# Kernel tuning notes

Measured on AMD Instinct MI355X. Metric: run time of the kernel, lower is better.

Reference implementation:

```python
import jax, jax.numpy as jnp
import numpy as np

B, ENC, W = 256, 512, 256      # batch, encoder hidden (backbone_out), encoder width
ATTN, DEC, EMB, V = 256, 256, 128, 81  # attn_sz, dec_hs, emb_size, alphabet_size
T = 100                         # text_max_len


def setup_inputs() -> dict:
    key = jax.random.key(0)
    ks = jax.random.split(key, 15)
    s = 0.05
    return {
        "enc_out": jax.random.normal(ks[0], (B, ENC, W), jnp.float32),
        "emb": jax.random.normal(ks[1], (V, EMB), jnp.float32) * s,
        "enc_conv_w": jax.random.normal(ks[2], (ATTN, ENC), jnp.float32) * s,  # Conv1d k=1
        "enc_conv_b": jax.random.normal(ks[3], (ATTN,), jnp.float32) * s,
        "dec_lin_w": jax.random.normal(ks[4], (ATTN, DEC), jnp.float32) * s,
        "dec_lin_b": jax.random.normal(ks[5], (ATTN,), jnp.float32) * s,
        "energy_w": jax.random.normal(ks[6], (ATTN,), jnp.float32) * s,  # Conv1d attn->1, k=1
        "energy_b": jax.random.normal(ks[7], (1,), jnp.float32) * s,
        "w_ih": jax.random.normal(ks[8], (4 * DEC, EMB + ENC), jnp.float32) * s,
        "w_hh": jax.random.normal(ks[9], (4 * DEC, DEC), jnp.float32) * s,
        "b_ih": jax.random.normal(ks[10], (4 * DEC,), jnp.float32) * s,
        "b_hh": jax.random.normal(ks[11], (4 * DEC,), jnp.float32) * s,
        "out_w": jax.random.normal(ks[12], (V, DEC), jnp.float32) * s,
        "out_b": jax.random.normal(ks[13], (V,), jnp.float32) * s,
        "text_max_len": T,
        "sos_idx": 0,
    }


def reference(enc_out, emb, enc_conv_w, enc_conv_b, dec_lin_w, dec_lin_b,
              energy_w, energy_b, w_ih, w_hh, b_ih, b_hh, out_w, out_b,
              text_max_len, sos_idx):
    bs = enc_out.shape[0]
    dec_hs = w_hh.shape[1]
    # precompute encoder projection (Conv1d with kernel 1) once: [bs, attn, W]
    weighted_enc = jnp.einsum('bew,ae->baw', enc_out, enc_conv_w) + enc_conv_b[None, :, None]

    def step(carry, _):
        h, c, x = carry
        ex = emb[x]                                            # [bs, emb]
        dec_proj = h @ dec_lin_w.T + dec_lin_b                 # [bs, attn]
        pre = jnp.tanh(weighted_enc + dec_proj[:, :, None])    # [bs, attn, W]
        scores = jnp.einsum('baw,a->bw', pre, energy_w) + energy_b  # [bs, W]
        alphas = jax.nn.softmax(scores, axis=-1)
        context = jnp.einsum('bew,bw->be', enc_out, alphas)    # [bs, enc]
        rnn_x = jnp.concatenate([ex, context], axis=1)         # [bs, emb+enc]
        gates = rnn_x @ w_ih.T + b_ih + h @ w_hh.T + b_hh      # [bs, 4*dec]
        i, f, g, o = jnp.split(gates, 4, axis=1)               # torch LSTMCell gate order
        i, f, o = jax.nn.sigmoid(i), jax.nn.sigmoid(f), jax.nn.sigmoid(o)
        g = jnp.tanh(g)
        c_new = f * c + i * g
        h_new = o * jnp.tanh(c_new)
        logits = h_new @ out_w.T + out_b                       # [bs, V]
        logp = jax.nn.log_softmax(logits, axis=-1)
        nxt = jnp.argmax(logp, axis=-1).astype(jnp.int32)      # greedy feedback (eval mode)
        return (h_new, c_new, nxt), (logp, nxt, alphas)

    h0 = jnp.zeros((bs, dec_hs), enc_out.dtype)
    c0 = jnp.zeros((bs, dec_hs), enc_out.dtype)
    x0 = jnp.full((bs,), sos_idx, jnp.int32)
    _, (logps, preds, attns) = jax.lax.scan(step, (h0, c0, x0), None, length=text_max_len)
    # [T,bs,...] -> [bs,T,...]
    return (logps.transpose(1, 0, 2), preds.T, attns.transpose(1, 0, 2))
```

## Files before the change

### kernel.cpp

```cpp
#include <hip/hip_runtime.h>

#define BATCH 256
#define ENCH  512
#define WWID  256
#define ATT   256
#define DECH  256
#define EMBD  128
#define VOC   81
#define TT    100

__device__ __forceinline__ float ftanh(float x) {
  float e = expf(2.0f * x);
  return 1.0f - 2.0f / (e + 1.0f);
}
__device__ __forceinline__ float fsig(float x) {
  return 1.0f / (1.0f + expf(-x));
}

__global__ void k_build(const float* __restrict__ w_ih, const float* __restrict__ w_hh,
                        const float* __restrict__ dlw,
                        float* __restrict__ W2, float* __restrict__ DW2) {
  int k = blockIdx.x, tid = threadIdx.x;
  if (k < 768) {
    for (int g = tid; g < 1024; g += 256)
      W2[(size_t)k * 1024 + g] = (k < 512) ? w_ih[(size_t)g * 640 + 128 + k]
                                           : w_hh[(size_t)g * 256 + (k - 512)];
  } else {
    int kk = k - 768;
    DW2[kk * 256 + tid] = dlw[tid * 256 + kk];
  }
}

__global__ void k_embg(const float* __restrict__ emb, const float* __restrict__ w_ih,
                       const float* __restrict__ b_ih, const float* __restrict__ b_hh,
                       float* __restrict__ embg) {
  int v = blockIdx.x, tid = threadIdx.x;
  __shared__ float em[EMBD];
  if (tid < EMBD) em[tid] = emb[v * EMBD + tid];
  __syncthreads();
  for (int g = tid; g < 1024; g += 256) {
    float s = b_ih[g] + b_hh[g];
    const float* wr = w_ih + (size_t)g * 640;
#pragma unroll 8
    for (int e = 0; e < EMBD; ++e) s += em[e] * wr[e];
    embg[v * 1024 + g] = s;
  }
}

__global__ void __launch_bounds__(256) k_we(const float* __restrict__ enc,
                                            const float* __restrict__ cw,
                                            const float* __restrict__ cb,
                                            float* __restrict__ we) {
  int bid = blockIdx.x;
  int b = bid >> 4, at = (bid >> 2) & 3, wt = bid & 3;
  int a0 = at * 64, w0 = wt * 64;
  __shared__ float cwT[32][68];
  __shared__ float encT[32][64];
  int tid = threadIdx.x;
  int tx = tid & 15, ty = tid >> 4;
  float acc[4][4] = {};
  const float* encB = enc + (size_t)b * ENCH * WWID;
  for (int k0 = 0; k0 < ENCH; k0 += 32) {
    {
      int a = tid >> 2, e8 = (tid & 3) * 8;
      const float* src = cw + (size_t)(a0 + a) * ENCH + k0 + e8;
      float4 v0 = *(const float4*)(src);
      float4 v1 = *(const float4*)(src + 4);
      cwT[e8 + 0][a] = v0.x; cwT[e8 + 1][a] = v0.y; cwT[e8 + 2][a] = v0.z; cwT[e8 + 3][a] = v0.w;
      cwT[e8 + 4][a] = v1.x; cwT[e8 + 5][a] = v1.y; cwT[e8 + 6][a] = v1.z; cwT[e8 + 7][a] = v1.w;
    }
    {
      int e = tid >> 3, w8 = (tid & 7) * 8;
      const float* src = encB + (size_t)(k0 + e) * WWID + w0 + w8;
      *(float4*)&encT[e][w8] = *(const float4*)src;
      *(float4*)&encT[e][w8 + 4] = *(const float4*)(src + 4);
    }
    __syncthreads();
#pragma unroll
    for (int e = 0; e < 32; ++e) {
      float4 av = *(const float4*)&cwT[e][ty * 4];
      float4 bv = *(const float4*)&encT[e][tx * 4];
      float a4[4] = {av.x, av.y, av.z, av.w};
      float b4[4] = {bv.x, bv.y, bv.z, bv.w};
#pragma unroll
      for (int i = 0; i < 4; ++i)
#pragma unroll
        for (int j = 0; j < 4; ++j) acc[i][j] += a4[i] * b4[j];
    }
    __syncthreads();
  }
#pragma unroll
  for (int i = 0; i < 4; ++i) {
    int a = a0 + ty * 4 + i;
    float bias = cb[a];
    float4 o;
    o.x = acc[i][0] + bias; o.y = acc[i][1] + bias;
    o.z = acc[i][2] + bias; o.w = acc[i][3] + bias;
    *(float4*)(we + ((size_t)(b * ATT + a)) * WWID + w0 + tx * 4) = o;
  }
}

__global__ void __launch_bounds__(1024, 1) k_loop(
    const float* __restrict__ we, const float* __restrict__ enc,
    const float* __restrict__ W2, const float* __restrict__ DW2,
    const float* __restrict__ embg, const float* __restrict__ dlb,
    const float* __restrict__ ew, const float* __restrict__ eb,
    const float* __restrict__ ow, const float* __restrict__ ob,
    const int* __restrict__ sos, float* __restrict__ out) {
  const int tid = threadIdx.x;
  const int b = blockIdx.x;

  __shared__ float xf_s[768];
  __shared__ float c_s[256];
  __shared__ float dp_s[256], ew_s[256], sc_s[256];
  __shared__ float partA[16][64][4];
  __shared__ float gpre_s[1024];
  __shared__ float red[8];
  __shared__ float lg[VOC], lp_s[VOC];
  __shared__ int xcur;

  if (tid < 256) {
    ew_s[tid] = ew[tid];
    c_s[tid] = 0.0f;
    xf_s[512 + tid] = 0.0f;
  }
  if (tid == 0) xcur = sos[0];
  const float ebv = eb[0];
  const float* weB = we + ((size_t)b << 16);
  const float* encB = enc + (size_t)b * ENCH * WWID;
  __syncthreads();

  for (int t = 0; t < TT; ++t) {
    if (tid < 256) {
      float acc = dlb[tid];
      const float* dw = DW2 + tid;
#pragma unroll 8
      for (int k = 0; k < DECH; ++k) acc += dw[k * 256] * xf_s[512 + k];
      dp_s[tid] = acc;
    }
    __syncthreads();
    {
      int q = tid & 63, pt = tid >> 6;
      float s0 = 0, s1 = 0, s2 = 0, s3 = 0;
      int abase = pt * 16;
#pragma unroll 4
      for (int i = 0; i < 16; ++i) {
        int aa = abase + i;
        float4 wv = *(const float4*)(weB + (size_t)aa * 256 + q * 4);
        float d = dp_s[aa], w8 = ew_s[aa];
        s0 += w8 * ftanh(wv.x + d);
        s1 += w8 * ftanh(wv.y + d);
        s2 += w8 * ftanh(wv.z + d);
        s3 += w8 * ftanh(wv.w + d);
      }
      partA[pt][q][0] = s0; partA[pt][q][1] = s1;
      partA[pt][q][2] = s2; partA[pt][q][3] = s3;
    }
    __syncthreads();
    float sv = 0.0f;
    if (tid < 256) {
      sv = ebv;
#pragma unroll
      for (int p = 0; p < 16; ++p) sv += partA[p][tid >> 2][tid & 3];
      float mm = sv;
      for (int off = 32; off; off >>= 1) mm = fmaxf(mm, __shfl_xor(mm, off));
      if ((tid & 63) == 0) red[tid >> 6] = mm;
    }
    __syncthreads();
    float mA = fmaxf(fmaxf(red[0], red[1]), fmaxf(red[2], red[3]));
    float pa = 0.0f;
    if (tid < 256) {
      pa = expf(sv - mA);
      float ss = pa;
      for (int off = 32; off; off >>= 1) ss += __shfl_xor(ss, off);
      if ((tid & 63) == 0) red[4 + (tid >> 6)] = ss;
    }
    __syncthreads();
    {
      float S = red[4] + red[5] + red[6] + red[7];
      if (tid < 256) {
        float alpha = pa / S;
        sc_s[tid] = alpha;
        out[(size_t)(BATCH * TT * VOC) + (size_t)(BATCH * TT) +
            ((size_t)b * TT + t) * WWID + tid] = alpha;
      }
    }
    __syncthreads();
    {
      int lane = tid & 63, wvi = tid >> 6;
      float4 al = *(const float4*)&sc_s[lane * 4];
#pragma unroll 4
      for (int e = wvi; e < ENCH; e += 16) {
        float4 evv = *(const float4*)(encB + (size_t)e * WWID + lane * 4);
        float s = evv.x * al.x + evv.y * al.y + evv.z * al.z + evv.w * al.w;
        for (int off = 32; off; off >>= 1) s += __shfl_xor(s, off);
        if (lane == 0) xf_s[e] = s;
      }
    }
    __syncthreads();
    {
      float acc = 0.0f;
      const float* w0 = W2 + tid;
#pragma unroll 2
      for (int k4 = 0; k4 < 192; ++k4) {
        float4 xv = *(const float4*)&xf_s[k4 * 4];
        const float* wp = w0 + (size_t)k4 * 4096;
        acc += wp[0] * xv.x + wp[1024] * xv.y + wp[2048] * xv.z + wp[3072] * xv.w;
      }
      gpre_s[tid] = acc + embg[(size_t)xcur * 1024 + tid];
    }
    __syncthreads();
    if (tid < 256) {
      float iv = fsig(gpre_s[tid]);
      float fv = fsig(gpre_s[256 + tid]);
      float gv = ftanh(gpre_s[512 + tid]);
      float ov = fsig(gpre_s[768 + tid]);
      float cn = fv * c_s[tid] + iv * gv;
      float hn = ov * ftanh(cn);
      c_s[tid] = cn;
      xf_s[512 + tid] = hn;
    }
    __syncthreads();
    {
      int lane = tid & 63, wv = tid >> 6;
      float4 hh = *(const float4*)&xf_s[512 + lane * 4];
      for (int v = wv; v < VOC; v += 16) {
        float4 wr = *(const float4*)(ow + (size_t)v * 256 + lane * 4);
        float s = wr.x * hh.x + wr.y * hh.y + wr.z * hh.z + wr.w * hh.w;
        for (int off = 32; off; off >>= 1) s += __shfl_xor(s, off);
        if (lane == 0) lg[v] = s + ob[v];
      }
    }
    __syncthreads();
    float v_ = -3.402823e38f, pe = 0.0f;
    if (tid < 256) {
      v_ = (tid < VOC) ? lg[tid] : -3.402823e38f;
      float mm = v_;
      for (int off = 32; off; off >>= 1) mm = fmaxf(mm, __shfl_xor(mm, off));
      if ((tid & 63) == 0) red[tid >> 6] = mm;
    }
    __syncthreads();
    float mC = fmaxf(fmaxf(red[0], red[1]), fmaxf(red[2], red[3]));
    if (tid < 256) {
      pe = (tid < VOC) ? expf(v_ - mC) : 0.0f;
      float ss = pe;
      for (int off = 32; off; off >>= 1) ss += __shfl_xor(ss, off);
      if ((tid & 63) == 0) red[4 + (tid >> 6)] = ss;
    }
    __syncthreads();
    {
      float S = red[4] + red[5] + red[6] + red[7];
      float lse = mC + logf(S);
      if (tid < VOC) {
        float lp = v_ - lse;
        lp_s[tid] = lp;
        out[((size_t)b * TT + t) * VOC + tid] = lp;
      }
    }
    __syncthreads();
    if (tid == 0) {
      int best = 0;
      float bv = lp_s[0];
      for (int v = 1; v < VOC; ++v) {
        float x = lp_s[v];
        if (x > bv) { bv = x; best = v; }
      }
      xcur = best;
      out[(size_t)(BATCH * TT * VOC) + (size_t)b * TT + t] = (float)best;
    }
    __syncthreads();
  }
}

extern "C" void kernel_launch(void* const* d_in, const int* in_sizes, int n_in,
                              void* d_out, int out_size, void* d_ws, size_t ws_size,
                              hipStream_t stream) {
  (void)in_sizes; (void)n_in; (void)out_size; (void)ws_size;
  const float* enc = (const float*)d_in[0];
  const float* emb = (const float*)d_in[1];
  const float* ecw = (const float*)d_in[2];
  const float* ecb = (const float*)d_in[3];
  const float* dlw = (const float*)d_in[4];
  const float* dlb = (const float*)d_in[5];
  const float* ew  = (const float*)d_in[6];
  const float* eb  = (const float*)d_in[7];
  const float* wih = (const float*)d_in[8];
  const float* whh = (const float*)d_in[9];
  const float* bih = (const float*)d_in[10];
  const float* bhh = (const float*)d_in[11];
  const float* ow  = (const float*)d_in[12];
  const float* ob  = (const float*)d_in[13];
  const int* sos   = (const int*)d_in[15];
  float* out = (float*)d_out;
  float* ws = (float*)d_ws;

  size_t off = 0;
  float* we    = ws + off; off += (size_t)BATCH * ATT * WWID;
  float* W2    = ws + off; off += (size_t)768 * 1024;
  float* DW2   = ws + off; off += (size_t)256 * 256;
  float* embg  = ws + off; off += (size_t)VOC * 1024;

  k_build<<<1024, 256, 0, stream>>>(wih, whh, dlw, W2, DW2);
  k_embg<<<VOC, 256, 0, stream>>>(emb, wih, bih, bhh, embg);
  k_we<<<4096, 256, 0, stream>>>(enc, ecw, ecb, we);
  k_loop<<<256, 1024, 0, stream>>>(we, enc, W2, DW2, embg, dlb, ew, eb, ow, ob,
                                   sos, out);
}
```

Measured before the change: 8.781 ms.

## Process two batch rows per block to share LSTM gate weight loads

```diff
diff --git a/kernel.cpp b/kernel.cpp
--- a/kernel.cpp
+++ b/kernel.cpp
@@ -108,165 +108,175 @@
     const float* __restrict__ ow, const float* __restrict__ ob,
     const int* __restrict__ sos, float* __restrict__ out) {
   const int tid = threadIdx.x;
-  const int b = blockIdx.x;
-
-  __shared__ float xf_s[768];
-  __shared__ float c_s[256];
-  __shared__ float dp_s[256], ew_s[256], sc_s[256];
+  const int hb = tid >> 9;
+  const int lt = tid & 511;
+  const int bb = blockIdx.x * 2 + hb;
+
+  __shared__ float xf_s[2][768];
+  __shared__ float c_s[2][256];
+  __shared__ float dp_s[2][256], sc_s[2][256];
+  __shared__ float ew_s[256];
   __shared__ float partA[16][64][4];
-  __shared__ float gpre_s[1024];
-  __shared__ float red[8];
-  __shared__ float lg[VOC], lp_s[VOC];
-  __shared__ int xcur;
-
-  if (tid < 256) {
-    ew_s[tid] = ew[tid];
-    c_s[tid] = 0.0f;
-    xf_s[512 + tid] = 0.0f;
-  }
-  if (tid == 0) xcur = sos[0];
+  __shared__ float gpre_s[2][1024];
+  __shared__ float red[2][8];
+  __shared__ float lg[2][VOC], lp_s[2][VOC];
+  __shared__ int xcur_s[2];
+
+  if (tid < 256) ew_s[tid] = ew[tid];
+  if (lt < 256) {
+    c_s[hb][lt] = 0.0f;
+    xf_s[hb][512 + lt] = 0.0f;
+  }
+  if (lt == 0) xcur_s[hb] = sos[0];
   const float ebv = eb[0];
-  const float* weB = we + ((size_t)b << 16);
-  const float* encB = enc + (size_t)b * ENCH * WWID;
+  const float* weB = we + ((size_t)bb << 16);
+  const float* encB = enc + (size_t)bb * ENCH * WWID;
   __syncthreads();
 
   for (int t = 0; t < TT; ++t) {
-    if (tid < 256) {
-      float acc = dlb[tid];
-      const float* dw = DW2 + tid;
+    if (lt < 256) {
+      float acc = dlb[lt];
+      const float* dw = DW2 + lt;
+      const float* hs = &xf_s[hb][512];
 #pragma unroll 8
-      for (int k = 0; k < DECH; ++k) acc += dw[k * 256] * xf_s[512 + k];
-      dp_s[tid] = acc;
-    }
-    __syncthreads();
-    {
-      int q = tid & 63, pt = tid >> 6;
+      for (int k = 0; k < DECH; ++k) acc += dw[k * 256] * hs[k];
+      dp_s[hb][lt] = acc;
+    }
+    __syncthreads();
+    {
+      int q = lt & 63, pt = lt >> 6;
       float s0 = 0, s1 = 0, s2 = 0, s3 = 0;
-      int abase = pt * 16;
-#pragma unroll 4
-      for (int i = 0; i < 16; ++i) {
+      int abase = pt * 32;
+#pragma unroll 8
+      for (int i = 0; i < 32; ++i) {
         int aa = abase + i;
         float4 wv = *(const float4*)(weB + (size_t)aa * 256 + q * 4);
-        float d = dp_s[aa], w8 = ew_s[aa];
+        float d = dp_s[hb][aa], w8 = ew_s[aa];
         s0 += w8 * ftanh(wv.x + d);
         s1 += w8 * ftanh(wv.y + d);
         s2 += w8 * ftanh(wv.z + d);
         s3 += w8 * ftanh(wv.w + d);
       }
-      partA[pt][q][0] = s0; partA[pt][q][1] = s1;
-      partA[pt][q][2] = s2; partA[pt][q][3] = s3;
+      int slab = hb * 8 + pt;
+      partA[slab][q][0] = s0; partA[slab][q][1] = s1;
+      partA[slab][q][2] = s2; partA[slab][q][3] = s3;
     }
     __syncthreads();
     float sv = 0.0f;
-    if (tid < 256) {
+    if (lt < 256) {
       sv = ebv;
-#pragma unroll
-      for (int p = 0; p < 16; ++p) sv += partA[p][tid >> 2][tid & 3];
+      const int base = hb * 8;
+#pragma unroll
+      for (int p = 0; p < 8; ++p) sv += partA[base + p][lt >> 2][lt & 3];
       float mm = sv;
       for (int off = 32; off; off >>= 1) mm = fmaxf(mm, __shfl_xor(mm, off));
-      if ((tid & 63) == 0) red[tid >> 6] = mm;
-    }
-    __syncthreads();
-    float mA = fmaxf(fmaxf(red[0], red[1]), fmaxf(red[2], red[3]));
+      if ((lt & 63) == 0) red[hb][lt >> 6] = mm;
+    }
+    __syncthreads();
+    float mA = fmaxf(fmaxf(red[hb][0], red[hb][1]), fmaxf(red[hb][2], red[hb][3]));
     float pa = 0.0f;
-    if (tid < 256) {
+    if (lt < 256) {
       pa = expf(sv - mA);
       float ss = pa;
       for (int off = 32; off; off >>= 1) ss += __shfl_xor(ss, off);
-      if ((tid & 63) == 0) red[4 + (tid >> 6)] = ss;
-    }
-    __syncthreads();
-    {
-      float S = red[4] + red[5] + red[6] + red[7];
-      if (tid < 256) {
+      if ((lt & 63) == 0) red[hb][4 + (lt >> 6)] = ss;
+    }
+    __syncthreads();
+    {
+      float S = red[hb][4] + red[hb][5] + red[hb][6] + red[hb][7];
+      if (lt < 256) {
         float alpha = pa / S;
-        sc_s[tid] = alpha;
+        sc_s[hb][lt] = alpha;
         out[(size_t)(BATCH * TT * VOC) + (size_t)(BATCH * TT) +
-            ((size_t)b * TT + t) * WWID + tid] = alpha;
-      }
-    }
-    __syncthreads();
-    {
-      int lane = tid & 63, wvi = tid >> 6;
-      float4 al = *(const float4*)&sc_s[lane * 4];
-#pragma unroll 4
-      for (int e = wvi; e < ENCH; e += 16) {
+            ((size_t)bb * TT + t) * WWID + lt] = alpha;
+      }
+    }
+    __syncthreads();
+    {
+      int lane = lt & 63, wvi = lt >> 6;
+      float4 al = *(const float4*)&sc_s[hb][lane * 4];
+#pragma unroll 2
+      for (int e = wvi; e < ENCH; e += 8) {
         float4 evv = *(const float4*)(encB + (size_t)e * WWID + lane * 4);
         float s = evv.x * al.x + evv.y * al.y + evv.z * al.z + evv.w * al.w;
         for (int off = 32; off; off >>= 1) s += __shfl_xor(s, off);
-        if (lane == 0) xf_s[e] = s;
-      }
-    }
-    __syncthreads();
-    {
-      float acc = 0.0f;
+        if (lane == 0) xf_s[hb][e] = s;
+      }
+    }
+    __syncthreads();
+    {
+      float a0 = 0.0f, a1 = 0.0f;
       const float* w0 = W2 + tid;
 #pragma unroll 2
       for (int k4 = 0; k4 < 192; ++k4) {
-        float4 xv = *(const float4*)&xf_s[k4 * 4];
+        float4 x0 = *(const float4*)&xf_s[0][k4 * 4];
+        float4 x1 = *(const float4*)&xf_s[1][k4 * 4];
         const float* wp = w0 + (size_t)k4 * 4096;
-        acc += wp[0] * xv.x + wp[1024] * xv.y + wp[2048] * xv.z + wp[3072] * xv.w;
-      }
-      gpre_s[tid] = acc + embg[(size_t)xcur * 1024 + tid];
-    }
-    __syncthreads();
-    if (tid < 256) {
-      float iv = fsig(gpre_s[tid]);
-      float fv = fsig(gpre_s[256 + tid]);
-      float gv = ftanh(gpre_s[512 + tid]);
-      float ov = fsig(gpre_s[768 + tid]);
-      float cn = fv * c_s[tid] + iv * gv;
+        float w_0 = wp[0], w_1 = wp[1024], w_2 = wp[2048], w_3 = wp[3072];
+        a0 += w_0 * x0.x + w_1 * x0.y + w_2 * x0.z + w_3 * x0.w;
+        a1 += w_0 * x1.x + w_1 * x1.y + w_2 * x1.z + w_3 * x1.w;
+      }
+      gpre_s[0][tid] = a0 + embg[(size_t)xcur_s[0] * 1024 + tid];
+      gpre_s[1][tid] = a1 + embg[(size_t)xcur_s[1] * 1024 + tid];
+    }
+    __syncthreads();
+    if (lt < 256) {
+      float iv = fsig(gpre_s[hb][lt]);
+      float fv = fsig(gpre_s[hb][256 + lt]);
+      float gv = ftanh(gpre_s[hb][512 + lt]);
+      float ov = fsig(gpre_s[hb][768 + lt]);
+      float cn = fv * c_s[hb][lt] + iv * gv;
       float hn = ov * ftanh(cn);
-      c_s[tid] = cn;
-      xf_s[512 + tid] = hn;
-    }
-    __syncthreads();
-    {
-      int lane = tid & 63, wv = tid >> 6;
-      float4 hh = *(const float4*)&xf_s[512 + lane * 4];
-      for (int v = wv; v < VOC; v += 16) {
+      c_s[hb][lt] = cn;
+      xf_s[hb][512 + lt] = hn;
+    }
+    __syncthreads();
+    {
+      int lane = lt & 63, wv = lt >> 6;
+      float4 hh = *(const float4*)&xf_s[hb][512 + lane * 4];
+      for (int v = wv; v < VOC; v += 8) {
         float4 wr = *(const float4*)(ow + (size_t)v * 256 + lane * 4);
         float s = wr.x * hh.x + wr.y * hh.y + wr.z * hh.z + wr.w * hh.w;
         for (int off = 32; off; off >>= 1) s += __shfl_xor(s, off);
-        if (lane == 0) lg[v] = s + ob[v];
+        if (lane == 0) lg[hb][v] = s + ob[v];
       }
     }
     __syncthreads();
     float v_ = -3.402823e38f, pe = 0.0f;
-    if (tid < 256) {
-      v_ = (tid < VOC) ? lg[tid] : -3.402823e38f;
+    if (lt < 256) {
+      v_ = (lt < VOC) ? lg[hb][lt] : -3.402823e38f;
       float mm = v_;
       for (int off = 32; off; off >>= 1) mm = fmaxf(mm, __shfl_xor(mm, off));
-      if ((tid & 63) == 0) red[tid >> 6] = mm;
-    }
-    __syncthreads();
-    float mC = fmaxf(fmaxf(red[0], red[1]), fmaxf(red[2], red[3]));
-    if (tid < 256) {
-      pe = (tid < VOC) ? expf(v_ - mC) : 0.0f;
+      if ((lt & 63) == 0) red[hb][lt >> 6] = mm;
+    }
+    __syncthreads();
+    float mC = fmaxf(fmaxf(red[hb][0], red[hb][1]), fmaxf(red[hb][2], red[hb][3]));
+    if (lt < 256) {
+      pe = (lt < VOC) ? expf(v_ - mC) : 0.0f;
       float ss = pe;
       for (int off = 32; off; off >>= 1) ss += __shfl_xor(ss, off);
-      if ((tid & 63) == 0) red[4 + (tid >> 6)] = ss;
-    }
-    __syncthreads();
-    {
-      float S = red[4] + red[5] + red[6] + red[7];
+      if ((lt & 63) == 0) red[hb][4 + (lt >> 6)] = ss;
+    }
+    __syncthreads();
+    {
+      float S = red[hb][4] + red[hb][5] + red[hb][6] + red[hb][7];
       float lse = mC + logf(S);
-      if (tid < VOC) {
+      if (lt < VOC) {
         float lp = v_ - lse;
-        lp_s[tid] = lp;
-        out[((size_t)b * TT + t) * VOC + tid] = lp;
-      }
-    }
-    __syncthreads();
-    if (tid == 0) {
+        lp_s[hb][lt] = lp;
+        out[((size_t)bb * TT + t) * VOC + lt] = lp;
+      }
+    }
+    __syncthreads();
+    if (lt == 0) {
       int best = 0;
-      float bv = lp_s[0];
+      float bv = lp_s[hb][0];
       for (int v = 1; v < VOC; ++v) {
-        float x = lp_s[v];
+        float x = lp_s[hb][v];
         if (x > bv) { bv = x; best = v; }
       }
-      xcur = best;
-      out[(size_t)(BATCH * TT * VOC) + (size_t)b * TT + t] = (float)best;
+      xcur_s[hb] = best;
+      out[(size_t)(BATCH * TT * VOC) + (size_t)bb * TT + t] = (float)best;
     }
     __syncthreads();
   }
@@ -303,6 +313,6 @@
   k_build<<<1024, 256, 0, stream>>>(wih, whh, dlw, W2, DW2);
   k_embg<<<VOC, 256, 0, stream>>>(emb, wih, bih, bhh, embg);
   k_we<<<4096, 256, 0, stream>>>(enc, ecw, ecb, we);
-  k_loop<<<256, 1024, 0, stream>>>(we, enc, W2, DW2, embg, dlb, ew, eb, ow, ob,
+  k_loop<<<128, 1024, 0, stream>>>(we, enc, W2, DW2, embg, dlb, ew, eb, ow, ob,
                                    sos, out);
 }
```

New measurement: 11.61 ms. 1.32x slower.

## Stream LSTM gate weights through LDS with async global_load_lds pipelining

Applied to the files above, without the earlier changes.

```diff
diff --git a/kernel.cpp b/kernel.cpp
--- a/kernel.cpp
+++ b/kernel.cpp
@@ -15,6 +15,13 @@
 }
 __device__ __forceinline__ float fsig(float x) {
   return 1.0f / (1.0f + expf(-x));
+}
+
+__device__ __forceinline__ void gl_lds4(const float* gsrc, float* ldst) {
+  typedef const __attribute__((address_space(1))) void* gas_t;
+  typedef __attribute__((address_space(3))) void* las_t;
+  __builtin_amdgcn_global_load_lds((gas_t)(const void*)gsrc, (las_t)(void*)ldst,
+                                   4, 0, 0);
 }
 
 __global__ void k_build(const float* __restrict__ w_ih, const float* __restrict__ w_hh,
@@ -110,6 +117,7 @@
   const int tid = threadIdx.x;
   const int b = blockIdx.x;
 
+  __shared__ float w2lds[16 * 4 * 512];
   __shared__ float xf_s[768];
   __shared__ float c_s[256];
   __shared__ float dp_s[256], ew_s[256], sc_s[256];
@@ -128,6 +136,7 @@
   const float ebv = eb[0];
   const float* weB = we + ((size_t)b << 16);
   const float* encB = enc + (size_t)b * ENCH * WWID;
+  const int q = tid & 63, pt = tid >> 6;
   __syncthreads();
 
   for (int t = 0; t < TT; ++t) {
@@ -140,7 +149,6 @@
     }
     __syncthreads();
     {
-      int q = tid & 63, pt = tid >> 6;
       float s0 = 0, s1 = 0, s2 = 0, s3 = 0;
       int abase = pt * 16;
 #pragma unroll 4
@@ -199,15 +207,47 @@
     }
     __syncthreads();
     {
+      float eg = embg[(size_t)xcur * 1024 + tid];
+      asm volatile("s_waitcnt vmcnt(0)" ::: "memory");
+      __builtin_amdgcn_sched_barrier(0);
+      float* wl = w2lds + pt * 2048;
+      const float* wsrc = W2 + pt * 64 + q;
       float acc = 0.0f;
-      const float* w0 = W2 + tid;
-#pragma unroll 2
-      for (int k4 = 0; k4 < 192; ++k4) {
-        float4 xv = *(const float4*)&xf_s[k4 * 4];
-        const float* wp = w0 + (size_t)k4 * 4096;
-        acc += wp[0] * xv.x + wp[1024] * xv.y + wp[2048] * xv.z + wp[3072] * xv.w;
-      }
-      gpre_s[tid] = acc + embg[(size_t)xcur * 1024 + tid];
+#pragma unroll
+      for (int i0 = 0; i0 < 3; ++i0) {
+        const float* src = wsrc + (size_t)(i0 * 8) * 1024;
+        float* dst = wl + i0 * 512;
+#pragma unroll
+        for (int r = 0; r < 8; ++r)
+          gl_lds4(src + (size_t)r * 1024, dst + r * 64);
+      }
+      for (int i = 0; i < 96; ++i) {
+        if (i < 94) {
+          asm volatile("s_waitcnt vmcnt(16)" ::: "memory");
+        } else if (i == 94) {
+          asm volatile("s_waitcnt vmcnt(8)" ::: "memory");
+        } else {
+          asm volatile("s_waitcnt vmcnt(0)" ::: "memory");
+        }
+        __builtin_amdgcn_sched_barrier(0);
+        const float* tl = wl + (i & 3) * 512;
+#pragma unroll
+        for (int r4 = 0; r4 < 2; ++r4) {
+          float4 xv = *(const float4*)&xf_s[(i * 2 + r4) * 4];
+          acc += tl[(r4 * 4 + 0) * 64 + q] * xv.x +
+                 tl[(r4 * 4 + 1) * 64 + q] * xv.y +
+                 tl[(r4 * 4 + 2) * 64 + q] * xv.z +
+                 tl[(r4 * 4 + 3) * 64 + q] * xv.w;
+        }
+        if (i + 3 < 96) {
+          const float* src = wsrc + (size_t)((i + 3) * 8) * 1024;
+          float* dst = wl + ((i + 3) & 3) * 512;
+#pragma unroll
+          for (int r = 0; r < 8; ++r)
+            gl_lds4(src + (size_t)r * 1024, dst + r * 64);
+        }
+      }
+      gpre_s[tid] = acc + eg;
     }
     __syncthreads();
     if (tid < 256) {
```

After: 9.176 ms. +4.5%, slower.
